# Kernel tuning notes

Hardware: AMD Instinct MI355X
Metric: run time of the kernel (lower is better)

Reference implementation:

```python
import jax, jax.numpy as jnp
import numpy as np
import math

B, S, H = 2, 4096, 512
NUM_HEADS = 8
HEAD_DIM = H // NUM_HEADS
RECENCY_DECAY = 0.9


def setup_inputs() -> dict:
    key = jax.random.key(0)
    k1, k2, k3 = jax.random.split(key, 3)
    scale = 1.0 / math.sqrt(H)
    x = jax.random.normal(k1, (B, S, H), dtype=jnp.float32)
    w_qkv = jax.random.normal(k2, (3 * H, H), dtype=jnp.float32) * scale
    w_out = jax.random.normal(k3, (H, H), dtype=jnp.float32) * scale
    b_out = jnp.zeros((H,), dtype=jnp.float32)
    return {"x": x, "w_qkv": w_qkv, "w_out": w_out, "b_out": b_out}


def reference(x, w_qkv, w_out, b_out):
    batch, seq_len, hidden = x.shape
    nh, hd = NUM_HEADS, HEAD_DIM
    # qkv projection (no bias): torch Linear computes x @ W.T
    qkv = jnp.einsum('bsh,oh->bso', x, w_qkv)
    qkv = qkv.reshape(batch, seq_len, 3, nh, hd)
    q, k, v = jnp.transpose(qkv, (2, 0, 3, 1, 4))  # each [B, nh, S, hd]
    attn = jnp.einsum('bhqd,bhkd->bhqk', q, k) / math.sqrt(hd)
    # recency bias: positions[i, j] = j - i; bias = (j-i)*log(decay) for j<=i else 0
    pos = jnp.arange(seq_len)[None, :] - jnp.arange(seq_len)[:, None]
    bias = jnp.where(pos <= 0, pos.astype(jnp.float32) * math.log(RECENCY_DECAY),
                     jnp.zeros((), dtype=jnp.float32))
    attn = jax.nn.softmax(attn + bias[None, None, :, :], axis=-1)
    out = jnp.einsum('bhqk,bhkd->bqhd', attn, v).reshape(batch, seq_len, hidden)
    return jnp.einsum('bsh,oh->bso', out, w_out) + b_out
```

## Files before the change

kernel.cpp:

```cpp
#include <hip/hip_runtime.h>
#include <hip/hip_bf16.h>
#include <stdint.h>

#define B_   2
#define S_   4096
#define H_   512
#define NH_  8
#define HD_  64
#define M_   (B_*S_)
#define LOG2D (-0.15200309344504997f)
#define SC2   (0.18033688011112042f)

#define NFULL        4
#define NCHUNK       8

typedef __attribute__((ext_vector_type(8))) short bf16x8_t;
typedef __attribute__((ext_vector_type(4))) float f32x4_t;

__device__ __forceinline__ void gl_lds16(const __hip_bfloat16* g, __hip_bfloat16* l) {
  __builtin_amdgcn_global_load_lds(
      (__attribute__((address_space(1))) void*)(g),
      (__attribute__((address_space(3))) void*)(l),
      16, 0, 0);
}

__global__ __launch_bounds__(256)
void cast3_kernel(const float* __restrict__ x, const float* __restrict__ wq,
                  const float* __restrict__ wo,
                  __hip_bfloat16* __restrict__ xb, __hip_bfloat16* __restrict__ wqb,
                  __hip_bfloat16* __restrict__ wob) {
  const int N0 = M_ * H_;
  const int N1 = 3 * H_ * H_;
  int i4 = (blockIdx.x * blockDim.x + threadIdx.x) * 4;
  const float* src; __hip_bfloat16* dst; int off;
  if (i4 < N0)           { src = x;  dst = xb;  off = i4; }
  else if (i4 < N0 + N1) { src = wq; dst = wqb; off = i4 - N0; }
  else                   { src = wo; dst = wob; off = i4 - N0 - N1; }
  float4 v = *(const float4*)(src + off);
  ushort4 o;
  __hip_bfloat16 h;
  h = __float2bfloat16(v.x); o.x = *(unsigned short*)&h;
  h = __float2bfloat16(v.y); o.y = *(unsigned short*)&h;
  h = __float2bfloat16(v.z); o.z = *(unsigned short*)&h;
  h = __float2bfloat16(v.w); o.w = *(unsigned short*)&h;
  *(ushort4*)((unsigned short*)dst + off) = o;
}

template<int EPI>
__global__ __launch_bounds__(256)
void gemm_bt(const __hip_bfloat16* __restrict__ A,
             const __hip_bfloat16* __restrict__ Bw,
             int K,
             __hip_bfloat16* __restrict__ qb,
             __hip_bfloat16* __restrict__ kb,
             __hip_bfloat16* __restrict__ vtb,
             float* __restrict__ outp,
             const float* __restrict__ bias) {
  __shared__ alignas(16) __hip_bfloat16 sA[128*64];
  __shared__ alignas(16) __hip_bfloat16 sB[128*64];
  const int tid  = threadIdx.x;
  const int wave = tid >> 6, lane = tid & 63;
  const int quad = lane >> 4, l15 = lane & 15;
  const int wr = (wave >> 1) * 64, wc = (wave & 1) * 64;
  const int m0 = blockIdx.y * 128, n0 = blockIdx.x * 128;

  const int sub  = lane >> 3;
  const int plog = (lane & 7) ^ sub;

  f32x4_t acc[4][4] = {};

  for (int kt = 0; kt < K; kt += 64) {
    __syncthreads();
    #pragma unroll
    for (int cc = 0; cc < 4; cc++) {
      int c   = wave * 4 + cc;
      int row = c * 8 + sub;
      gl_lds16(A  + (size_t)(m0 + row) * K + kt + plog * 8, sA + c * 512);
      gl_lds16(Bw + (size_t)(n0 + row) * K + kt + plog * 8, sB + c * 512);
    }
    __syncthreads();
    #pragma unroll
    for (int kh = 0; kh < 2; kh++) {
      bf16x8_t af[4], bfr[4];
      #pragma unroll
      for (int x = 0; x < 4; x++) {
        int row = wr + x * 16 + l15;
        int pos = kh * 4 + quad;
        af[x] = *(const bf16x8_t*)(sA + row * 64 + ((pos ^ (row & 7)) << 3));
      }
      #pragma unroll
      for (int y = 0; y < 4; y++) {
        int row = wc + y * 16 + l15;
        int pos = kh * 4 + quad;
        bfr[y] = *(const bf16x8_t*)(sB + row * 64 + ((pos ^ (row & 7)) << 3));
      }
      #pragma unroll
      for (int x = 0; x < 4; x++)
        #pragma unroll
        for (int y = 0; y < 4; y++)
          acc[x][y] = __builtin_amdgcn_mfma_f32_16x16x32_bf16(af[x], bfr[y], acc[x][y], 0, 0, 0);
    }
  }

  if (EPI == 0 && (n0 >> 9) == 2) {
    #pragma unroll
    for (int x = 0; x < 4; x++) {
      int gr = m0 + wr + x * 16 + quad * 4;
      int bb = gr >> 12, sb = gr & 4095;
      #pragma unroll
      for (int y = 0; y < 4; y++) {
        int rem = (n0 - 1024) + wc + y * 16 + l15;
        int h = rem >> 6, d = rem & 63;
        ushort4 o; __hip_bfloat16 hv;
        hv = __float2bfloat16(acc[x][y][0]); o.x = *(unsigned short*)&hv;
        hv = __float2bfloat16(acc[x][y][1]); o.y = *(unsigned short*)&hv;
        hv = __float2bfloat16(acc[x][y][2]); o.z = *(unsigned short*)&hv;
        hv = __float2bfloat16(acc[x][y][3]); o.w = *(unsigned short*)&hv;
        *(ushort4*)(vtb + ((size_t)(bb * NH_ + h) * HD_ + d) * S_ + sb) = o;
      }
    }
  } else {
    #pragma unroll
    for (int x = 0; x < 4; x++) {
      #pragma unroll
      for (int y = 0; y < 4; y++) {
        #pragma unroll
        for (int r = 0; r < 4; r++) {
          int gr = m0 + wr + x*16 + quad*4 + r;
          int gc = n0 + wc + y*16 + l15;
          float v = acc[x][y][r];
          if (EPI == 0) {
            int bb = gr >> 12, s = gr & 4095;
            int t  = gc >> 9,  rem = gc & 511;
            int h  = rem >> 6, d = rem & 63;
            __hip_bfloat16 hv = __float2bfloat16(v);
            int bh = bb * NH_ + h;
            if (t == 0) qb[((size_t)bh * S_ + s) * HD_ + d] = hv;
            else        kb[((size_t)bh * S_ + s) * HD_ + d] = hv;
          } else {
            outp[(size_t)gr * H_ + gc] = v + bias[gc];
          }
        }
      }
    }
  }
}

__device__ __forceinline__ void stage_kv(const __hip_bfloat16* __restrict__ kb,
                                         const __hip_bfloat16* __restrict__ vtb,
                                         int bh, int j0,
                                         __hip_bfloat16* dK, __hip_bfloat16* dV,
                                         int wave, int lane) {
  const int subK  = lane >> 3;
  const int plogK = (lane & 7) ^ subK;
  const int subV  = lane >> 4;
  #pragma unroll
  for (int cc = 0; cc < 4; cc++) {
    int c = wave * 4 + cc;
    int rK = c * 8 + subK;
    gl_lds16(kb + ((size_t)bh * S_ + j0 + rK) * HD_ + plogK * 8, dK + c * 512);
    int rV = c * 4 + subV;
    int plogV = (lane & 15) ^ (rV & 15);
    gl_lds16(vtb + ((size_t)bh * HD_ + rV) * S_ + j0 + plogV * 8, dV + c * 512);
  }
}

__global__ __launch_bounds__(256)
void attn_kernel(const __hip_bfloat16* __restrict__ qb,
                 const __hip_bfloat16* __restrict__ kb,
                 const __hip_bfloat16* __restrict__ vtb,
                 __hip_bfloat16* __restrict__ ob,
                 float* __restrict__ pO,
                 float* __restrict__ pl) {
  __shared__ alignas(16) __hip_bfloat16 sK[128*64];
  __shared__ alignas(16) __hip_bfloat16 sV[64*128];
  __shared__ alignas(16) __hip_bfloat16 sP[4][16*128];

  const int tid  = threadIdx.x;
  const int wave = tid >> 6, lane = tid & 63;
  const int quad = lane >> 4, l15 = lane & 15;
  const int w  = blockIdx.x;
  const int bh = blockIdx.y;

  int q0, jt0, niter, chunk = 0;
  bool direct;
  if (w < 30) { q0 = 256 + w * 128; jt0 = 0; niter = 2; direct = true; }
  else { int t = w - 30; chunk = t & 7; q0 = (t >> 3) * 128; jt0 = chunk * 4; niter = 4; direct = false; }

  const int rgb0 = q0 + wave * 32;
  bf16x8_t aQ[2][2];
  #pragma unroll
  for (int g = 0; g < 2; g++) {
    const __hip_bfloat16* qrow = qb + ((size_t)bh * S_ + rgb0 + g * 16 + l15) * HD_;
    aQ[g][0] = *(const bf16x8_t*)(qrow + quad * 8);
    aQ[g][1] = *(const bf16x8_t*)(qrow + 32 + quad * 8);
  }

  f32x4_t accO[2][4] = {};
  float l_r[2][4];
  float negM2[2][4];
  #pragma unroll
  for (int g = 0; g < 2; g++)
    #pragma unroll
    for (int r = 0; r < 4; r++) {
      l_r[g][r] = 0.f;
      negM2[g][r] = -(17.312340f - LOG2D * (float)(rgb0 + g * 16 + quad * 4 + r));
    }

  __hip_bfloat16* sPw = &sP[wave][0];

  for (int it = 0; it < niter; ++it) {
    const int j0 = (jt0 + it) * 128;
    __syncthreads();
    stage_kv(kb, vtb, bh, j0, sK, sV, wave, lane);
    __syncthreads();

    #pragma unroll
    for (int g = 0; g < 2; ++g) {
      f32x4_t sfr[8];
      #pragma unroll
      for (int ni = 0; ni < 8; ni++) {
        int row = ni * 16 + l15;
        f32x4_t a = {};
        bf16x8_t b0 = *(const bf16x8_t*)(sK + row * 64 + ((quad       ^ (row & 7)) << 3));
        bf16x8_t b1 = *(const bf16x8_t*)(sK + row * 64 + (((quad + 4) ^ (row & 7)) << 3));
        a = __builtin_amdgcn_mfma_f32_16x16x32_bf16(aQ[g][0], b0, a, 0, 0, 0);
        a = __builtin_amdgcn_mfma_f32_16x16x32_bf16(aQ[g][1], b1, a, 0, 0, 0);
        sfr[ni] = a;
      }

      #pragma unroll
      for (int r = 0; r < 4; r++) {
        const float d0 = (float)(j0 + l15 - (rgb0 + g * 16 + quad * 4 + r));
        const int row = quad * 4 + r;
        float psum = 0.f;
        #pragma unroll
        for (int ni = 0; ni < 8; ni++) {
          float dij = d0 + (float)(ni * 16);
          float arg = fmaf(fminf(dij, 0.f), LOG2D, fmaf(sfr[ni][r], SC2, negM2[g][r]));
          float p = __builtin_amdgcn_exp2f(arg);
          psum += p;
          int col = ni * 16 + l15;
          sPw[row * 128 + (((col >> 3) ^ (row & 15)) << 3) + (col & 7)] = __float2bfloat16(p);
        }
        l_r[g][r] += psum;
      }
      __builtin_amdgcn_sched_barrier(0);
      __builtin_amdgcn_s_waitcnt(0xC07F);
      __builtin_amdgcn_sched_barrier(0);

      #pragma unroll
      for (int kk = 0; kk < 4; kk++) {
        int pos = kk * 4 + quad;
        bf16x8_t aP = *(const bf16x8_t*)(sPw + l15 * 128 + ((pos ^ l15) << 3));
        #pragma unroll
        for (int nd = 0; nd < 4; nd++) {
          int row = nd * 16 + l15;
          bf16x8_t bV = *(const bf16x8_t*)(sV + row * 128 + ((pos ^ (row & 15)) << 3));
          accO[g][nd] = __builtin_amdgcn_mfma_f32_16x16x32_bf16(aP, bV, accO[g][nd], 0, 0, 0);
        }
      }
      __builtin_amdgcn_sched_barrier(0);
    }
  }

  #pragma unroll
  for (int g = 0; g < 2; g++)
    #pragma unroll
    for (int r = 0; r < 4; r++) {
      float l = l_r[g][r];
      #pragma unroll
      for (int msk = 1; msk < 16; msk <<= 1) l += __shfl_xor(l, msk, 64);
      l_r[g][r] = l;
    }

  if (direct) {
    const int b = bh >> 3, h = bh & 7;
    #pragma unroll
    for (int g = 0; g < 2; g++)
      #pragma unroll
      for (int r = 0; r < 4; r++) {
        float invr = 1.0f / l_r[g][r];
        #pragma unroll
        for (int nd = 0; nd < 4; nd++) {
          int srow = rgb0 + g * 16 + quad * 4 + r;
          int col  = h * HD_ + nd * 16 + l15;
          ob[((size_t)b * S_ + srow) * H_ + col] = __float2bfloat16(accO[g][nd][r] * invr);
        }
      }
  } else {
    const int qt    = (q0 >> 6) + (wave >> 1);
    const int rbase = (wave & 1) * 32;
    size_t base = ((size_t)bh * NFULL + qt) * NCHUNK + chunk;
    float* po = pO + base * 4096;
    #pragma unroll
    for (int g = 0; g < 2; g++) {
      #pragma unroll
      for (int nd = 0; nd < 4; nd++)
        #pragma unroll
        for (int r = 0; r < 4; r++)
          po[(rbase + g*16 + quad*4 + r) * 64 + nd*16 + l15] = accO[g][nd][r];
      if (l15 == 0) {
        #pragma unroll
        for (int r = 0; r < 4; r++)
          pl[base * 64 + rbase + g*16 + quad*4 + r] = l_r[g][r];
      }
    }
  }
}

__global__ __launch_bounds__(256)
void combine_kernel(const float* __restrict__ pO,
                    const float* __restrict__ pl,
                    __hip_bfloat16* __restrict__ ob) {
  const int f  = blockIdx.x;
  const int bh = blockIdx.y;
  const int tid = threadIdx.x;
  const int rr = tid >> 2, cg = (tid & 3) * 16;
  const size_t base0 = ((size_t)bh * NFULL + f) * NCHUNK;

  float L = 0.f;
  #pragma unroll
  for (int c = 0; c < NCHUNK; c++) L += pl[(base0 + c) * 64 + rr];
  const float inv = 1.0f / L;

  float o[16];
  #pragma unroll
  for (int k = 0; k < 16; k++) o[k] = 0.f;
  #pragma unroll
  for (int c = 0; c < NCHUNK; c++) {
    const float4* src = (const float4*)(pO + (base0 + c) * 4096 + rr * 64 + cg);
    #pragma unroll
    for (int k4 = 0; k4 < 4; k4++) {
      float4 v = src[k4];
      o[k4*4+0] += v.x; o[k4*4+1] += v.y;
      o[k4*4+2] += v.z; o[k4*4+3] += v.w;
    }
  }
  const int b = bh >> 3, h = bh & 7, s = f * 64 + rr;
  __hip_bfloat16* dst = ob + ((size_t)b * S_ + s) * H_ + h * HD_ + cg;
  #pragma unroll
  for (int k = 0; k < 16; k++) dst[k] = __float2bfloat16(o[k] * inv);
}

extern "C" void kernel_launch(void* const* d_in, const int* in_sizes, int n_in,
                              void* d_out, int out_size, void* d_ws, size_t ws_size,
                              hipStream_t stream) {
  const float* x     = (const float*)d_in[0];
  const float* w_qkv = (const float*)d_in[1];
  const float* w_out = (const float*)d_in[2];
  const float* b_out = (const float*)d_in[3];
  float* out = (float*)d_out;

  char* ws = (char*)d_ws;
  __hip_bfloat16* xb  = (__hip_bfloat16*)(ws);
  __hip_bfloat16* wqb = (__hip_bfloat16*)(ws + (8u  << 20));
  __hip_bfloat16* wob = (__hip_bfloat16*)(ws + (10u << 20));
  __hip_bfloat16* qb  = (__hip_bfloat16*)(ws + (11u << 20));
  __hip_bfloat16* kb  = (__hip_bfloat16*)(ws + (19u << 20));
  __hip_bfloat16* vtb = (__hip_bfloat16*)(ws + (27u << 20));
  float*          pO  = (float*)(ws + (36u << 20));
  float*          pl  = (float*)(ws + (49u << 20));
  __hip_bfloat16* ab  = xb;

  cast3_kernel<<<dim3(5120), dim3(256), 0, stream>>>(x, w_qkv, w_out, xb, wqb, wob);
  gemm_bt<0><<<dim3(12, 64), dim3(256), 0, stream>>>(xb, wqb, H_, qb, kb, vtb, nullptr, nullptr);
  attn_kernel<<<dim3(30 + 2 * NCHUNK, B_ * NH_), dim3(256), 0, stream>>>(qb, kb, vtb, ab, pO, pl);
  combine_kernel<<<dim3(NFULL, B_ * NH_), dim3(256), 0, stream>>>(pO, pl, ab);
  gemm_bt<1><<<dim3(4, 64), dim3(256), 0, stream>>>(ab, wob, H_, nullptr, nullptr, nullptr, out, b_out);
}
```

Baseline: 145.8 us.

## Halve attention block tile to 64 queries and 64-key steps, doubling grid size

The attention kernel now has each block cover 64 query rows (16 per wave) and iterate over 64-key tiles. The early query rows are split into 16 chunks instead of 8, and K/V staging is divided between waves. Grid size rises from 46 to 124 blocks per head, which targets under-filled CUs on a 256-CU part and lowers LDS use per block. In exchange, each block reloads K/V more often relative to its work, synchronises more often, and writes more partial results for the combine step.

```diff
diff --git a/kernel.cpp b/kernel.cpp
--- a/kernel.cpp
+++ b/kernel.cpp
@@ -12,7 +12,7 @@
 #define SC2   (0.18033688011112042f)
 
 #define NFULL        4
-#define NCHUNK       8
+#define NCHUNK       16
 
 typedef __attribute__((ext_vector_type(8))) short bf16x8_t;
 typedef __attribute__((ext_vector_type(4))) float f32x4_t;
@@ -146,25 +146,6 @@
   }
 }
 
-__device__ __forceinline__ void stage_kv(const __hip_bfloat16* __restrict__ kb,
-                                         const __hip_bfloat16* __restrict__ vtb,
-                                         int bh, int j0,
-                                         __hip_bfloat16* dK, __hip_bfloat16* dV,
-                                         int wave, int lane) {
-  const int subK  = lane >> 3;
-  const int plogK = (lane & 7) ^ subK;
-  const int subV  = lane >> 4;
-  #pragma unroll
-  for (int cc = 0; cc < 4; cc++) {
-    int c = wave * 4 + cc;
-    int rK = c * 8 + subK;
-    gl_lds16(kb + ((size_t)bh * S_ + j0 + rK) * HD_ + plogK * 8, dK + c * 512);
-    int rV = c * 4 + subV;
-    int plogV = (lane & 15) ^ (rV & 15);
-    gl_lds16(vtb + ((size_t)bh * HD_ + rV) * S_ + j0 + plogV * 8, dV + c * 512);
-  }
-}
-
 __global__ __launch_bounds__(256)
 void attn_kernel(const __hip_bfloat16* __restrict__ qb,
                  const __hip_bfloat16* __restrict__ kb,
@@ -172,9 +153,9 @@
                  __hip_bfloat16* __restrict__ ob,
                  float* __restrict__ pO,
                  float* __restrict__ pl) {
-  __shared__ alignas(16) __hip_bfloat16 sK[128*64];
-  __shared__ alignas(16) __hip_bfloat16 sV[64*128];
-  __shared__ alignas(16) __hip_bfloat16 sP[4][16*128];
+  __shared__ alignas(16) __hip_bfloat16 sK[64*64];
+  __shared__ alignas(16) __hip_bfloat16 sV[64*64];
+  __shared__ alignas(16) __hip_bfloat16 sP[4][16*64];
 
   const int tid  = threadIdx.x;
   const int wave = tid >> 6, lane = tid & 63;
@@ -182,129 +163,124 @@
   const int w  = blockIdx.x;
   const int bh = blockIdx.y;
 
-  int q0, jt0, niter, chunk = 0;
+  int q0, jt0, chunk = 0;
   bool direct;
-  if (w < 30) { q0 = 256 + w * 128; jt0 = 0; niter = 2; direct = true; }
-  else { int t = w - 30; chunk = t & 7; q0 = (t >> 3) * 128; jt0 = chunk * 4; niter = 4; direct = false; }
-
-  const int rgb0 = q0 + wave * 32;
-  bf16x8_t aQ[2][2];
-  #pragma unroll
-  for (int g = 0; g < 2; g++) {
-    const __hip_bfloat16* qrow = qb + ((size_t)bh * S_ + rgb0 + g * 16 + l15) * HD_;
-    aQ[g][0] = *(const bf16x8_t*)(qrow + quad * 8);
-    aQ[g][1] = *(const bf16x8_t*)(qrow + 32 + quad * 8);
-  }
-
-  f32x4_t accO[2][4] = {};
-  float l_r[2][4];
-  float negM2[2][4];
-  #pragma unroll
-  for (int g = 0; g < 2; g++)
+  if (w < 60) { q0 = 256 + w * 64; jt0 = 0; direct = true; }
+  else { int t = w - 60; chunk = t & 15; q0 = (t >> 4) * 64; jt0 = chunk * 4; direct = false; }
+
+  const __hip_bfloat16* qrow = qb + ((size_t)bh * S_ + q0 + wave * 16 + l15) * HD_;
+  bf16x8_t aQ0 = *(const bf16x8_t*)(qrow + quad * 8);
+  bf16x8_t aQ1 = *(const bf16x8_t*)(qrow + 32 + quad * 8);
+
+  f32x4_t accO[4] = {};
+  float l_r[4], negM2[4];
+  const int row_i = q0 + wave * 16 + quad * 4;
+  #pragma unroll
+  for (int r = 0; r < 4; r++) {
+    l_r[r] = 0.f;
+    negM2[r] = -(17.312340f - LOG2D * (float)(row_i + r));
+  }
+
+  const int sub  = lane >> 3;
+  const int plog = (lane & 7) ^ sub;
+  __hip_bfloat16* sPw = &sP[wave][0];
+
+  for (int it = 0; it < 4; ++it) {
+    const int j0 = (jt0 + it) * 64;
+    __syncthreads();
+    if (wave < 2) {
+      #pragma unroll
+      for (int cc = 0; cc < 4; cc++) {
+        int c = wave * 4 + cc;
+        gl_lds16(kb + ((size_t)bh * S_ + j0 + c * 8 + sub) * HD_ + plog * 8, sK + c * 512);
+      }
+    } else {
+      #pragma unroll
+      for (int cc = 0; cc < 4; cc++) {
+        int c = (wave - 2) * 4 + cc;
+        gl_lds16(vtb + ((size_t)bh * HD_ + c * 8 + sub) * S_ + j0 + plog * 8, sV + c * 512);
+      }
+    }
+    __syncthreads();
+
+    f32x4_t sfr[4];
+    #pragma unroll
+    for (int ni = 0; ni < 4; ni++) {
+      int row = ni * 16 + l15;
+      f32x4_t a = {};
+      bf16x8_t b0 = *(const bf16x8_t*)(sK + row * 64 + ((quad       ^ (row & 7)) << 3));
+      bf16x8_t b1 = *(const bf16x8_t*)(sK + row * 64 + (((quad + 4) ^ (row & 7)) << 3));
+      a = __builtin_amdgcn_mfma_f32_16x16x32_bf16(aQ0, b0, a, 0, 0, 0);
+      a = __builtin_amdgcn_mfma_f32_16x16x32_bf16(aQ1, b1, a, 0, 0, 0);
+      sfr[ni] = a;
+    }
+
     #pragma unroll
     for (int r = 0; r < 4; r++) {
-      l_r[g][r] = 0.f;
-      negM2[g][r] = -(17.312340f - LOG2D * (float)(rgb0 + g * 16 + quad * 4 + r));
-    }
-
-  __hip_bfloat16* sPw = &sP[wave][0];
-
-  for (int it = 0; it < niter; ++it) {
-    const int j0 = (jt0 + it) * 128;
-    __syncthreads();
-    stage_kv(kb, vtb, bh, j0, sK, sV, wave, lane);
-    __syncthreads();
-
-    #pragma unroll
-    for (int g = 0; g < 2; ++g) {
-      f32x4_t sfr[8];
-      #pragma unroll
-      for (int ni = 0; ni < 8; ni++) {
-        int row = ni * 16 + l15;
-        f32x4_t a = {};
-        bf16x8_t b0 = *(const bf16x8_t*)(sK + row * 64 + ((quad       ^ (row & 7)) << 3));
-        bf16x8_t b1 = *(const bf16x8_t*)(sK + row * 64 + (((quad + 4) ^ (row & 7)) << 3));
-        a = __builtin_amdgcn_mfma_f32_16x16x32_bf16(aQ[g][0], b0, a, 0, 0, 0);
-        a = __builtin_amdgcn_mfma_f32_16x16x32_bf16(aQ[g][1], b1, a, 0, 0, 0);
-        sfr[ni] = a;
-      }
-
-      #pragma unroll
-      for (int r = 0; r < 4; r++) {
-        const float d0 = (float)(j0 + l15 - (rgb0 + g * 16 + quad * 4 + r));
-        const int row = quad * 4 + r;
-        float psum = 0.f;
-        #pragma unroll
-        for (int ni = 0; ni < 8; ni++) {
-          float dij = d0 + (float)(ni * 16);
-          float arg = fmaf(fminf(dij, 0.f), LOG2D, fmaf(sfr[ni][r], SC2, negM2[g][r]));
-          float p = __builtin_amdgcn_exp2f(arg);
-          psum += p;
-          int col = ni * 16 + l15;
-          sPw[row * 128 + (((col >> 3) ^ (row & 15)) << 3) + (col & 7)] = __float2bfloat16(p);
-        }
-        l_r[g][r] += psum;
-      }
-      __builtin_amdgcn_sched_barrier(0);
-      __builtin_amdgcn_s_waitcnt(0xC07F);
-      __builtin_amdgcn_sched_barrier(0);
-
-      #pragma unroll
-      for (int kk = 0; kk < 4; kk++) {
-        int pos = kk * 4 + quad;
-        bf16x8_t aP = *(const bf16x8_t*)(sPw + l15 * 128 + ((pos ^ l15) << 3));
-        #pragma unroll
-        for (int nd = 0; nd < 4; nd++) {
-          int row = nd * 16 + l15;
-          bf16x8_t bV = *(const bf16x8_t*)(sV + row * 128 + ((pos ^ (row & 15)) << 3));
-          accO[g][nd] = __builtin_amdgcn_mfma_f32_16x16x32_bf16(aP, bV, accO[g][nd], 0, 0, 0);
-        }
-      }
-      __builtin_amdgcn_sched_barrier(0);
-    }
-  }
-
-  #pragma unroll
-  for (int g = 0; g < 2; g++)
-    #pragma unroll
-    for (int r = 0; r < 4; r++) {
-      float l = l_r[g][r];
-      #pragma unroll
-      for (int msk = 1; msk < 16; msk <<= 1) l += __shfl_xor(l, msk, 64);
-      l_r[g][r] = l;
-    }
+      const float d0 = (float)(j0 + l15 - (row_i + r));
+      const int row = quad * 4 + r;
+      float psum = 0.f;
+      #pragma unroll
+      for (int ni = 0; ni < 4; ni++) {
+        float dij = d0 + (float)(ni * 16);
+        float arg = fmaf(fminf(dij, 0.f), LOG2D, fmaf(sfr[ni][r], SC2, negM2[r]));
+        float p = __builtin_amdgcn_exp2f(arg);
+        psum += p;
+        int col = ni * 16 + l15;
+        sPw[row * 64 + (((col >> 3) ^ (row & 7)) << 3) + (col & 7)] = __float2bfloat16(p);
+      }
+      l_r[r] += psum;
+    }
+    __builtin_amdgcn_sched_barrier(0);
+    __builtin_amdgcn_s_waitcnt(0xC07F);
+    __builtin_amdgcn_sched_barrier(0);
+
+    bf16x8_t aP0 = *(const bf16x8_t*)(sPw + l15 * 64 + ((quad       ^ (l15 & 7)) << 3));
+    bf16x8_t aP1 = *(const bf16x8_t*)(sPw + l15 * 64 + (((quad + 4) ^ (l15 & 7)) << 3));
+    #pragma unroll
+    for (int nd = 0; nd < 4; nd++) {
+      int row = nd * 16 + l15;
+      bf16x8_t b0 = *(const bf16x8_t*)(sV + row * 64 + ((quad       ^ (row & 7)) << 3));
+      bf16x8_t b1 = *(const bf16x8_t*)(sV + row * 64 + (((quad + 4) ^ (row & 7)) << 3));
+      accO[nd] = __builtin_amdgcn_mfma_f32_16x16x32_bf16(aP0, b0, accO[nd], 0, 0, 0);
+      accO[nd] = __builtin_amdgcn_mfma_f32_16x16x32_bf16(aP1, b1, accO[nd], 0, 0, 0);
+    }
+    __builtin_amdgcn_sched_barrier(0);
+  }
+
+  #pragma unroll
+  for (int r = 0; r < 4; r++) {
+    float l = l_r[r];
+    #pragma unroll
+    for (int msk = 1; msk < 16; msk <<= 1) l += __shfl_xor(l, msk, 64);
+    l_r[r] = l;
+  }
 
   if (direct) {
     const int b = bh >> 3, h = bh & 7;
     #pragma unroll
-    for (int g = 0; g < 2; g++)
-      #pragma unroll
-      for (int r = 0; r < 4; r++) {
-        float invr = 1.0f / l_r[g][r];
-        #pragma unroll
-        for (int nd = 0; nd < 4; nd++) {
-          int srow = rgb0 + g * 16 + quad * 4 + r;
-          int col  = h * HD_ + nd * 16 + l15;
-          ob[((size_t)b * S_ + srow) * H_ + col] = __float2bfloat16(accO[g][nd][r] * invr);
-        }
-      }
+    for (int r = 0; r < 4; r++) {
+      float invr = 1.0f / l_r[r];
+      #pragma unroll
+      for (int nd = 0; nd < 4; nd++) {
+        int srow = q0 + wave * 16 + quad * 4 + r;
+        int col  = h * HD_ + nd * 16 + l15;
+        ob[((size_t)b * S_ + srow) * H_ + col] = __float2bfloat16(accO[nd][r] * invr);
+      }
+    }
   } else {
-    const int qt    = (q0 >> 6) + (wave >> 1);
-    const int rbase = (wave & 1) * 32;
+    const int qt = q0 >> 6;
     size_t base = ((size_t)bh * NFULL + qt) * NCHUNK + chunk;
     float* po = pO + base * 4096;
     #pragma unroll
-    for (int g = 0; g < 2; g++) {
-      #pragma unroll
-      for (int nd = 0; nd < 4; nd++)
-        #pragma unroll
-        for (int r = 0; r < 4; r++)
-          po[(rbase + g*16 + quad*4 + r) * 64 + nd*16 + l15] = accO[g][nd][r];
-      if (l15 == 0) {
-        #pragma unroll
-        for (int r = 0; r < 4; r++)
-          pl[base * 64 + rbase + g*16 + quad*4 + r] = l_r[g][r];
-      }
+    for (int nd = 0; nd < 4; nd++)
+      #pragma unroll
+      for (int r = 0; r < 4; r++)
+        po[(wave*16 + quad*4 + r) * 64 + nd*16 + l15] = accO[nd][r];
+    if (l15 == 0) {
+      #pragma unroll
+      for (int r = 0; r < 4; r++)
+        pl[base * 64 + wave*16 + quad*4 + r] = l_r[r];
     }
   }
 }
@@ -360,12 +336,12 @@
   __hip_bfloat16* kb  = (__hip_bfloat16*)(ws + (19u << 20));
   __hip_bfloat16* vtb = (__hip_bfloat16*)(ws + (27u << 20));
   float*          pO  = (float*)(ws + (36u << 20));
-  float*          pl  = (float*)(ws + (49u << 20));
+  float*          pl  = (float*)(ws + (53u << 20));
   __hip_bfloat16* ab  = xb;
 
   cast3_kernel<<<dim3(5120), dim3(256), 0, stream>>>(x, w_qkv, w_out, xb, wqb, wob);
   gemm_bt<0><<<dim3(12, 64), dim3(256), 0, stream>>>(xb, wqb, H_, qb, kb, vtb, nullptr, nullptr);
-  attn_kernel<<<dim3(30 + 2 * NCHUNK, B_ * NH_), dim3(256), 0, stream>>>(qb, kb, vtb, ab, pO, pl);
+  attn_kernel<<<dim3(60 + NFULL * NCHUNK, B_ * NH_), dim3(256), 0, stream>>>(qb, kb, vtb, ab, pO, pl);
   combine_kernel<<<dim3(NFULL, B_ * NH_), dim3(256), 0, stream>>>(pO, pl, ab);
   gemm_bt<1><<<dim3(4, 64), dim3(256), 0, stream>>>(ab, wob, H_, nullptr, nullptr, nullptr, out, b_out);
 }
```

New measurement: 143.8 us. No clear change (-1.3%).
